# Performance work log

Measured on AMD Instinct MI355X. Metric: run time of the kernel, lower is better.

The kernel has to match this reference:

```python
import jax, jax.numpy as jnp
import numpy as np

CHANNELS = 768
N_HEADS = 12
HEAD_DIM = CHANNELS // N_HEADS
WINDOW = 4
B, T = 4, 1024


def setup_inputs() -> dict:
    key = jax.random.key(0)
    ks = jax.random.split(key, 11)
    C = CHANNELS
    s = 1.0 / np.sqrt(C)
    inp = {
        "x": jax.random.normal(ks[0], (B, C, T), dtype=jnp.float32),
        "w_q": jax.random.normal(ks[1], (C, C), dtype=jnp.float32) * s,
        "b_q": jnp.zeros((C,), dtype=jnp.float32),
        "w_k": jax.random.normal(ks[2], (C, C), dtype=jnp.float32) * s,
        "b_k": jnp.zeros((C,), dtype=jnp.float32),
        "w_v": jax.random.normal(ks[3], (C, C), dtype=jnp.float32) * s,
        "b_v": jnp.zeros((C,), dtype=jnp.float32),
        "w_o": jax.random.normal(ks[4], (C, C), dtype=jnp.float32) * s,
        "b_o": jnp.zeros((C,), dtype=jnp.float32),
        "emb_rel_k": jax.random.normal(ks[5], (2 * WINDOW + 1, HEAD_DIM), dtype=jnp.float32) * 0.01,
        "emb_rel_v": jax.random.normal(ks[6], (2 * WINDOW + 1, HEAD_DIM), dtype=jnp.float32) * 0.01,
    }
    return inp


def _rel_embeddings(emb_k, emb_v, t):
    pos = jnp.arange(t)
    rel_pos = pos[None, :] - pos[:, None]            # (T, T), rel_pos[i,j] = j - i
    outside = jnp.abs(rel_pos) > WINDOW
    rel_idx = jnp.clip(rel_pos, -WINDOW, WINDOW) + WINDOW
    rel_k = jnp.where(outside[:, :, None], 0.0, emb_k[rel_idx])  # (T, T, d)
    rel_v = jnp.where(outside[:, :, None], 0.0, emb_v[rel_idx])
    return rel_k, rel_v


def reference(x, w_q, b_q, w_k, b_k, w_v, b_v, w_o, b_o, emb_rel_k, emb_rel_v):
    Bq, C, t = x.shape
    H, d = N_HEADS, HEAD_DIM
    # 1x1 Conv1d == per-timestep linear over channels
    def proj(w, b):
        return jnp.einsum('oc,bct->bot', w, x) + b[None, :, None]
    # (B, C, T) -> (B, H, T, d)
    def split_heads(y):
        return y.reshape(Bq, H, d, t).transpose(0, 1, 3, 2)
    q = split_heads(proj(w_q, b_q)) / jnp.sqrt(jnp.float32(d))
    k = split_heads(proj(w_k, b_k))
    v = split_heads(proj(w_v, b_v))
    scores = jnp.einsum('bhid,bhjd->bhij', q, k)
    rel_k, rel_v = _rel_embeddings(emb_rel_k, emb_rel_v, t)
    scores = scores + jnp.einsum('bhid,ijd->bhij', q, rel_k)
    attn = jax.nn.softmax(scores, axis=-1)
    out = jnp.einsum('bhij,bhjd->bhid', attn, v)
    out = out + jnp.einsum('bhij,ijd->bhid', attn, rel_v)
    out = out.transpose(0, 1, 3, 2).reshape(Bq, C, t)  # (B, C, T)
    out = jnp.einsum('oc,bct->bot', w_o, out) + b_o[None, :, None]
    return out
```

## Files before the change

kernel.cpp:

```cpp
#include <hip/hip_runtime.h>

#define B_ 4
#define T_ 1024
#define C_ 768
#define H_ 12
#define D_ 64

typedef unsigned short u16;
typedef __attribute__((ext_vector_type(8))) short b16x8;
typedef __attribute__((ext_vector_type(4))) float f32x4;

#define MFMA(a, b, c) __builtin_amdgcn_mfma_f32_16x16x32_bf16(a, b, c, 0, 0, 0)

__device__ __forceinline__ float b2f(u16 u) {
    return __uint_as_float(((unsigned)u) << 16);
}
__device__ __forceinline__ u16 f2b(float f) {
    unsigned u = __float_as_uint(f);
    u += 0x7fffu + ((u >> 16) & 1u);
    return (u16)(u >> 16);
}
__device__ __forceinline__ u16 f2b_tr(float f) {
    return (u16)(__float_as_uint(f) >> 16);
}

__device__ __forceinline__ void g2l16(const u16* g, u16* l) {
    __builtin_amdgcn_global_load_lds(
        (const __attribute__((address_space(1))) unsigned int*)g,
        (__attribute__((address_space(3))) unsigned int*)l, 16, 0, 0);
}

__global__ __launch_bounds__(256) void convw_kernel(
    const float* __restrict__ w0, const float* __restrict__ w1,
    const float* __restrict__ w2, const float* __restrict__ w3,
    u16* __restrict__ o)
{
    const float* src = blockIdx.y == 0 ? w0 : blockIdx.y == 1 ? w1 :
                       blockIdx.y == 2 ? w2 : w3;
    u16* dst = o + (size_t)blockIdx.y * C_ * C_;
    const int i = (blockIdx.x * 256 + threadIdx.x) * 4;
    float4 v = *(const float4*)(src + i);
    ushort4 st = {f2b(v.x), f2b(v.y), f2b(v.z), f2b(v.w)};
    *(ushort4*)(dst + i) = st;
}

__global__ __launch_bounds__(256) void convx_kernel(
    const float* __restrict__ x, u16* __restrict__ xb)
{
    __shared__ u16 tile[64][68];
    const int tid = threadIdx.x;
    const int t0 = blockIdx.x * 64, c0 = blockIdx.y * 64, b = blockIdx.z;
    #pragma unroll
    for (int p = 0; p < 4; ++p) {
        const int cc = p * 16 + (tid >> 4);
        const int t4 = (tid & 15) * 4;
        float4 v = *(const float4*)(x + ((size_t)b * C_ + c0 + cc) * T_ + t0 + t4);
        tile[t4 + 0][cc] = f2b(v.x);
        tile[t4 + 1][cc] = f2b(v.y);
        tile[t4 + 2][cc] = f2b(v.z);
        tile[t4 + 3][cc] = f2b(v.w);
    }
    __syncthreads();
    #pragma unroll
    for (int p = 0; p < 4; ++p) {
        const int tt = p * 16 + (tid >> 4);
        const int c4 = (tid & 15) * 4;
        ushort4 st = *(const ushort4*)&tile[tt][c4];
        *(ushort4*)(xb + ((size_t)b * T_ + t0 + tt) * C_ + c0 + c4) = st;
    }
}

__global__ __launch_bounds__(256) void qkv_mfma_kernel(
    const u16* __restrict__ wb, const u16* __restrict__ xb,
    const float* __restrict__ b_q, const float* __restrict__ b_k,
    const float* __restrict__ b_v,
    u16* __restrict__ q_ws, u16* __restrict__ k_ws, u16* __restrict__ v_ws)
{
    __shared__ __align__(16) u16 a_s[128 * 32];
    __shared__ __align__(16) u16 b_s[128 * 32];

    const int tid = threadIdx.x;
    const int wv = tid >> 6, lane = tid & 63;
    const int lo = lane & 15, quad = lane >> 4;
    const int wm = wv >> 1, wn = wv & 1;
    const int swz = (lo >> 1) & 3;
    const int srow = lane >> 2;
    const int skb  = (lane & 3) ^ ((lane >> 3) & 3);

    const int t0 = blockIdx.x * 128;
    const int mat = blockIdx.y / 6, oy = blockIdx.y % 6;
    const int o0 = oy * 128;
    const int b  = blockIdx.z;

    const u16* A = wb + (size_t)mat * C_ * C_;
    const float* bias = mat == 0 ? b_q : (mat == 1 ? b_k : b_v);
    u16* dst = mat == 0 ? q_ws : (mat == 1 ? k_ws : v_ws);
    const float scale = mat == 0 ? 0.18033688f : 1.0f;

    const size_t bT0 = (size_t)b * T_ + t0;

    f32x4 acc[4][4] = {};

    for (int kk = 0; kk < C_; kk += 32) {
        __syncthreads();
        #pragma unroll
        for (int ia = 0; ia < 2; ++ia) {
            const int row0 = (wv * 2 + ia) * 16;
            g2l16(A + (size_t)(o0 + row0 + srow) * C_ + kk + skb * 8,
                  a_s + row0 * 32);
        }
        #pragma unroll
        for (int ib = 0; ib < 2; ++ib) {
            const int row0 = (wv * 2 + ib) * 16;
            g2l16(xb + (bT0 + row0 + srow) * C_ + kk + skb * 8,
                  b_s + row0 * 32);
        }
        __syncthreads();

        b16x8 af[4], bf[4];
        #pragma unroll
        for (int mi = 0; mi < 4; ++mi) {
            const int m = wm * 64 + mi * 16 + lo;
            af[mi] = *(const b16x8*)(a_s + m * 32 + (quad ^ swz) * 8);
        }
        #pragma unroll
        for (int ni = 0; ni < 4; ++ni) {
            const int n = wn * 64 + ni * 16 + lo;
            bf[ni] = *(const b16x8*)(b_s + n * 32 + (quad ^ swz) * 8);
        }
        #pragma unroll
        for (int mi = 0; mi < 4; ++mi)
            #pragma unroll
            for (int ni = 0; ni < 4; ++ni)
                acc[mi][ni] = MFMA(af[mi], bf[ni], acc[mi][ni]);
    }

    #pragma unroll
    for (int mi = 0; mi < 4; ++mi) {
        const int o_b = o0 + wm * 64 + mi * 16 + quad * 4;
        const float4 bv4 = *(const float4*)(bias + o_b);
        const int h = o_b >> 6;
        const int dd0 = o_b & 63;
        #pragma unroll
        for (int ni = 0; ni < 4; ++ni) {
            const int t = t0 + wn * 64 + ni * 16 + lo;
            f32x4 a = acc[mi][ni];
            ushort4 st;
            st.x = f2b((a[0] + bv4.x) * scale);
            st.y = f2b((a[1] + bv4.y) * scale);
            st.z = f2b((a[2] + bv4.z) * scale);
            st.w = f2b((a[3] + bv4.w) * scale);
            *(ushort4*)(dst + (((size_t)b * H_ + h) * T_ + t) * D_ + dd0) = st;
        }
    }
}

__global__ __launch_bounds__(256) void transv_kernel(
    const u16* __restrict__ src, u16* __restrict__ dst)
{
    __shared__ __align__(16) u16 tile[64 * 72];
    const int tid = threadIdx.x;
    const int t0 = blockIdx.x * 64;
    const int bh = blockIdx.y;
    const u16* s = src + (size_t)bh * T_ * D_;
    u16* d = dst + (size_t)bh * D_ * T_;
    #pragma unroll
    for (int p = 0; p < 2; ++p) {
        const int idx = tid + p * 256;
        const int row = idx >> 3, ch = idx & 7;
        *(b16x8*)(tile + row * 72 + ch * 8) =
            *(const b16x8*)(s + (size_t)(t0 + row) * D_ + ch * 8);
    }
    __syncthreads();
    #pragma unroll
    for (int p = 0; p < 2; ++p) {
        const int idx = tid + p * 256;
        const int dd = idx >> 3, ch = idx & 7;
        union { b16x8 v; u16 e[8]; } t;
        #pragma unroll
        for (int e = 0; e < 8; ++e)
            t.e[e] = tile[(ch * 8 + e) * 72 + dd];
        *(b16x8*)(d + (size_t)dd * T_ + t0 + ch * 8) = t.v;
    }
}

__global__ __launch_bounds__(256) void out_mfma_kernel(
    const u16* __restrict__ wob, const u16* __restrict__ ab,
    const float* __restrict__ bias, float* __restrict__ out)
{
    __shared__ __align__(16) u16 a_s[64 * 32];
    __shared__ __align__(16) u16 b_s[128 * 32];

    const int tid = threadIdx.x;
    const int wv = tid >> 6, lane = tid & 63;
    const int lo = lane & 15, quad = lane >> 4;
    const int wm = wv >> 1, wn = wv & 1;
    const int swz = (lo >> 1) & 3;
    const int srow = lane >> 2;
    const int skb  = (lane & 3) ^ ((lane >> 3) & 3);

    const int t0 = blockIdx.x * 128;
    const int o0 = blockIdx.y * 64;
    const int b  = blockIdx.z;
    const size_t bT0 = (size_t)b * T_ + t0;

    f32x4 acc[2][4] = {};

    for (int kk = 0; kk < C_; kk += 32) {
        __syncthreads();
        {
            const int row0 = wv * 16;
            g2l16(wob + (size_t)(o0 + row0 + srow) * C_ + kk + skb * 8,
                  a_s + row0 * 32);
        }
        #pragma unroll
        for (int ib = 0; ib < 2; ++ib) {
            const int row0 = (wv * 2 + ib) * 16;
            g2l16(ab + (bT0 + row0 + srow) * C_ + kk + skb * 8,
                  b_s + row0 * 32);
        }
        __syncthreads();

        b16x8 af[2], bf[4];
        #pragma unroll
        for (int mi = 0; mi < 2; ++mi) {
            const int m = wm * 32 + mi * 16 + lo;
            af[mi] = *(const b16x8*)(a_s + m * 32 + (quad ^ swz) * 8);
        }
        #pragma unroll
        for (int ni = 0; ni < 4; ++ni) {
            const int n = wn * 64 + ni * 16 + lo;
            bf[ni] = *(const b16x8*)(b_s + n * 32 + (quad ^ swz) * 8);
        }
        #pragma unroll
        for (int mi = 0; mi < 2; ++mi)
            #pragma unroll
            for (int ni = 0; ni < 4; ++ni)
                acc[mi][ni] = MFMA(af[mi], bf[ni], acc[mi][ni]);
    }

    #pragma unroll
    for (int mi = 0; mi < 2; ++mi) {
        const int o_b = o0 + wm * 32 + mi * 16 + quad * 4;
        const float4 bv4 = *(const float4*)(bias + o_b);
        const float bb[4] = {bv4.x, bv4.y, bv4.z, bv4.w};
        #pragma unroll
        for (int ni = 0; ni < 4; ++ni) {
            const int t = t0 + wn * 64 + ni * 16 + lo;
            f32x4 a = acc[mi][ni];
            #pragma unroll
            for (int r = 0; r < 4; ++r)
                out[((size_t)b * C_ + o_b + r) * T_ + t] = a[r] + bb[r];
        }
    }
}

__global__ __launch_bounds__(256, 2) void attn_mfma_kernel(
    const u16* __restrict__ qw, const u16* __restrict__ kw, const u16* __restrict__ vw,
    const float* __restrict__ erk, const float* __restrict__ erv,
    u16* __restrict__ att)
{
    __shared__ __align__(16) u16 k_s[64 * 64];
    __shared__ __align__(16) u16 v_s[64 * 64];
    __shared__ __align__(16) u16 p_s[64 * 64];
    __shared__ float qrel_s[64][9];
    __shared__ float band_s[64][9];
    __shared__ float linv_s[64];

    const int tid = threadIdx.x;
    const int wv = tid >> 6, lane = tid & 63;
    const int lo = lane & 15, quad = lane >> 4;
    const int wi0 = wv * 16;
    const int it0 = blockIdx.x * 64;
    const int h = blockIdx.y, b = blockIdx.z;
    const int bh = b * H_ + h;

    const u16* qp = qw + (size_t)bh * T_ * D_;
    const u16* kp = kw + (size_t)bh * T_ * D_;
    const u16* vp = vw + (size_t)bh * D_ * T_;

    const int srow = lane >> 3;
    const int schunk = (lane & 7) ^ srow;
    const int lsw = lo & 7;

    b16x8 qf[2];
    #pragma unroll
    for (int kc = 0; kc < 2; ++kc)
        qf[kc] = *(const b16x8*)(qp + (size_t)(it0 + wi0 + lo) * D_ + kc * 32 + quad * 8);

    {
        b16x8 ekf[2];
        #pragma unroll
        for (int kc = 0; kc < 2; ++kc) {
            union { b16x8 v; u16 s[8]; } t;
            #pragma unroll
            for (int r = 0; r < 8; ++r) t.s[r] = 0;
            if (lo < 9) {
                const float* e = erk + lo * D_ + kc * 32 + quad * 8;
                #pragma unroll
                for (int r = 0; r < 8; ++r) t.s[r] = f2b(e[r]);
            }
            ekf[kc] = t.v;
        }
        f32x4 acc = {};
        acc = MFMA(qf[0], ekf[0], acc);
        acc = MFMA(qf[1], ekf[1], acc);
        if (lo < 9)
            #pragma unroll
            for (int r = 0; r < 4; ++r)
                qrel_s[wi0 + quad * 4 + r][lo] = acc[r];
    }

    for (int idx = lane; idx < 16 * 9; idx += 64)
        band_s[wi0 + idx / 9][idx % 9] = -1e30f;

    f32x4 o[4] = {};
    float lpart = 0.f;

    for (int jt = 0; jt < T_; jt += 64) {
        __syncthreads();
        #pragma unroll
        for (int i2 = 0; i2 < 2; ++i2) {
            const int row0 = (wv * 2 + i2) * 8;
            g2l16(kp + (size_t)(jt + row0 + srow) * D_ + schunk * 8, k_s + row0 * 64);
            g2l16(vp + (size_t)(row0 + srow) * T_ + jt + schunk * 8, v_s + row0 * 64);
        }
        __syncthreads();

        f32x4 st[4];
        #pragma unroll
        for (int mt = 0; mt < 4; ++mt) {
            const int kr = mt * 16 + lo;
            const b16x8 ka0 = *(const b16x8*)(k_s + kr * 64 + ((quad) ^ lsw) * 8);
            const b16x8 ka1 = *(const b16x8*)(k_s + kr * 64 + ((4 + quad) ^ lsw) * 8);
            f32x4 a = {};
            a = MFMA(ka0, qf[0], a);
            a = MFMA(ka1, qf[1], a);
            st[mt] = a;
        }

        if (jt >= it0 - 67 && jt <= it0 + 67) {
            const int ibase = it0 + wi0 + lo;
            #pragma unroll
            for (int mt = 0; mt < 4; ++mt)
                #pragma unroll
                for (int r = 0; r < 4; ++r) {
                    const int rr = (jt + mt * 16 + quad * 4 + r) - ibase + 4;
                    if (rr >= 0 && rr <= 8) {
                        const float s2 = st[mt][r] + qrel_s[wi0 + lo][rr];
                        st[mt][r] = s2;
                        band_s[wi0 + lo][rr] = s2;
                    }
                }
        }

        #pragma unroll
        for (int mt = 0; mt < 4; ++mt)
            #pragma unroll
            for (int r = 0; r < 4; ++r) {
                const float e = exp2f(st[mt][r]);
                st[mt][r] = e;
                lpart += e;
            }

        #pragma unroll
        for (int mt = 0; mt < 4; ++mt) {
            ushort4 pw;
            pw.x = f2b_tr(st[mt][0]);
            pw.y = f2b_tr(st[mt][1]);
            pw.z = f2b_tr(st[mt][2]);
            pw.w = f2b_tr(st[mt][3]);
            const int slot = (mt * 2 + (quad >> 1)) ^ lsw;
            *(ushort4*)(p_s + (wi0 + lo) * 64 + slot * 8 + (quad & 1) * 4) = pw;
        }

        const b16x8 pa0 = *(const b16x8*)(p_s + (wi0 + lo) * 64 + ((quad) ^ lsw) * 8);
        const b16x8 pa1 = *(const b16x8*)(p_s + (wi0 + lo) * 64 + ((4 + quad) ^ lsw) * 8);
        #pragma unroll
        for (int nd = 0; nd < 4; ++nd) {
            const int vr = nd * 16 + lo;
            const b16x8 vb0 = *(const b16x8*)(v_s + vr * 64 + ((quad) ^ lsw) * 8);
            const b16x8 vb1 = *(const b16x8*)(v_s + vr * 64 + ((4 + quad) ^ lsw) * 8);
            o[nd] = MFMA(pa0, vb0, o[nd]);
            o[nd] = MFMA(pa1, vb1, o[nd]);
        }
    }

    {
        union { b16x8 v; u16 s[8]; } tb;
        #pragma unroll
        for (int r = 0; r < 8; ++r) {
            const int rr = quad * 8 + r;
            tb.s[r] = (rr <= 8) ? f2b(exp2f(band_s[wi0 + lo][rr])) : (u16)0;
        }
        const b16x8 baf = tb.v;
        #pragma unroll
        for (int nd = 0; nd < 4; ++nd) {
            union { b16x8 v; u16 s[8]; } t;
            #pragma unroll
            for (int r = 0; r < 8; ++r) {
                const int rr = quad * 8 + r;
                t.s[r] = (rr <= 8) ? f2b(erv[rr * D_ + nd * 16 + lo]) : (u16)0;
            }
            o[nd] = MFMA(baf, t.v, o[nd]);
        }
    }

    lpart += __shfl_xor(lpart, 16);
    lpart += __shfl_xor(lpart, 32);
    if (quad == 0) linv_s[wi0 + lo] = 1.f / lpart;
    #pragma unroll
    for (int r = 0; r < 4; ++r) {
        const int il = wi0 + quad * 4 + r;
        const float inv = linv_s[il];
        const size_t base = ((size_t)b * T_ + it0 + il) * C_ + h * D_;
        #pragma unroll
        for (int nd = 0; nd < 4; ++nd)
            att[base + nd * 16 + lo] = f2b(o[nd][r] * inv);
    }
}

extern "C" void kernel_launch(void* const* d_in, const int* in_sizes, int n_in,
                              void* d_out, int out_size, void* d_ws, size_t ws_size,
                              hipStream_t stream) {
    const float* x   = (const float*)d_in[0];
    const float* w_q = (const float*)d_in[1];
    const float* b_q = (const float*)d_in[2];
    const float* w_k = (const float*)d_in[3];
    const float* b_k = (const float*)d_in[4];
    const float* w_v = (const float*)d_in[5];
    const float* b_v = (const float*)d_in[6];
    const float* w_o = (const float*)d_in[7];
    const float* b_o = (const float*)d_in[8];
    const float* erk = (const float*)d_in[9];
    const float* erv = (const float*)d_in[10];

    const size_t N = (size_t)B_ * C_ * T_;
    u16* q_ws  = (u16*)d_ws;
    u16* k_ws  = q_ws + N;
    u16* vraw  = q_ws + 2 * N;
    u16* vdT   = q_ws + 3 * N;
    u16* xb    = q_ws + 4 * N;
    u16* a_ws  = vraw;
    u16* wb    = q_ws + 5 * N;
    float* out = (float*)d_out;

    dim3 blk(256, 1, 1);

    convw_kernel<<<dim3(C_ * C_ / 1024, 4), blk, 0, stream>>>(w_q, w_k, w_v, w_o, wb);
    convx_kernel<<<dim3(T_ / 64, C_ / 64, B_), blk, 0, stream>>>(x, xb);

    qkv_mfma_kernel<<<dim3(T_ / 128, 18, B_), blk, 0, stream>>>(
        wb, xb, b_q, b_k, b_v, q_ws, k_ws, vraw);

    transv_kernel<<<dim3(T_ / 64, H_ * B_), blk, 0, stream>>>(vraw, vdT);

    attn_mfma_kernel<<<dim3(T_ / 64, H_, B_), blk, 0, stream>>>(
        q_ws, k_ws, vdT, erk, erv, a_ws);

    out_mfma_kernel<<<dim3(T_ / 128, C_ / 64, B_), blk, 0, stream>>>(
        wb + 3 * (size_t)C_ * C_, a_ws, b_o, out);
}
```

Baseline: 170.2 us.

## Fuse conversion kernels, fold V transpose into QKV epilogue, enlarge out-proj tile

Merges the weight and input bf16 conversion kernels into one launch. The V transpose moves into the QKV GEMM epilogue, which stages the tile in shared memory and writes the transposed layout directly, removing the separate transpose kernel and its extra global round trip. The output projection tile grows from 64 to 128 output channels per block, which raises reuse but halves the grid to 192 blocks. The larger QKV shared buffer (128x136) may lower occupancy.

Result: slower. 176.0 us (+3.4%).

```diff
diff --git a/kernel.cpp b/kernel.cpp
--- a/kernel.cpp
+++ b/kernel.cpp
@@ -30,26 +30,30 @@
         (__attribute__((address_space(3))) unsigned int*)l, 16, 0, 0);
 }
 
-__global__ __launch_bounds__(256) void convw_kernel(
+__global__ __launch_bounds__(256) void conv_fused_kernel(
     const float* __restrict__ w0, const float* __restrict__ w1,
     const float* __restrict__ w2, const float* __restrict__ w3,
-    u16* __restrict__ o)
-{
-    const float* src = blockIdx.y == 0 ? w0 : blockIdx.y == 1 ? w1 :
-                       blockIdx.y == 2 ? w2 : w3;
-    u16* dst = o + (size_t)blockIdx.y * C_ * C_;
-    const int i = (blockIdx.x * 256 + threadIdx.x) * 4;
-    float4 v = *(const float4*)(src + i);
-    ushort4 st = {f2b(v.x), f2b(v.y), f2b(v.z), f2b(v.w)};
-    *(ushort4*)(dst + i) = st;
-}
-
-__global__ __launch_bounds__(256) void convx_kernel(
-    const float* __restrict__ x, u16* __restrict__ xb)
+    u16* __restrict__ wb, const float* __restrict__ x, u16* __restrict__ xb)
 {
     __shared__ u16 tile[64][68];
+    const int bx = blockIdx.x;
     const int tid = threadIdx.x;
-    const int t0 = blockIdx.x * 64, c0 = blockIdx.y * 64, b = blockIdx.z;
+
+    if (bx < 2304) {
+        const int mat = bx / 576;
+        const float* src = mat == 0 ? w0 : mat == 1 ? w1 : mat == 2 ? w2 : w3;
+        u16* dst = wb + (size_t)mat * C_ * C_;
+        const int i = ((bx % 576) * 256 + tid) * 4;
+        float4 v = *(const float4*)(src + i);
+        ushort4 st = {f2b(v.x), f2b(v.y), f2b(v.z), f2b(v.w)};
+        *(ushort4*)(dst + i) = st;
+        return;
+    }
+
+    const int cx = bx - 2304;
+    const int t0 = (cx & 15) * 64;
+    const int c0 = ((cx >> 4) % 12) * 64;
+    const int b  = cx / 192;
     #pragma unroll
     for (int p = 0; p < 4; ++p) {
         const int cc = p * 16 + (tid >> 4);
@@ -74,10 +78,11 @@
     const u16* __restrict__ wb, const u16* __restrict__ xb,
     const float* __restrict__ b_q, const float* __restrict__ b_k,
     const float* __restrict__ b_v,
-    u16* __restrict__ q_ws, u16* __restrict__ k_ws, u16* __restrict__ v_ws)
+    u16* __restrict__ q_ws, u16* __restrict__ k_ws, u16* __restrict__ vT_ws)
 {
-    __shared__ __align__(16) u16 a_s[128 * 32];
-    __shared__ __align__(16) u16 b_s[128 * 32];
+    __shared__ __align__(16) u16 smem[128 * 136];
+    u16* a_s = smem;
+    u16* b_s = smem + 128 * 32;
 
     const int tid = threadIdx.x;
     const int wv = tid >> 6, lane = tid & 63;
@@ -94,7 +99,6 @@
 
     const u16* A = wb + (size_t)mat * C_ * C_;
     const float* bias = mat == 0 ? b_q : (mat == 1 ? b_k : b_v);
-    u16* dst = mat == 0 ? q_ws : (mat == 1 ? k_ws : v_ws);
     const float scale = mat == 0 ? 0.18033688f : 1.0f;
 
     const size_t bT0 = (size_t)b * T_ + t0;
@@ -135,52 +139,52 @@
                 acc[mi][ni] = MFMA(af[mi], bf[ni], acc[mi][ni]);
     }
 
-    #pragma unroll
-    for (int mi = 0; mi < 4; ++mi) {
-        const int o_b = o0 + wm * 64 + mi * 16 + quad * 4;
-        const float4 bv4 = *(const float4*)(bias + o_b);
-        const int h = o_b >> 6;
-        const int dd0 = o_b & 63;
-        #pragma unroll
-        for (int ni = 0; ni < 4; ++ni) {
-            const int t = t0 + wn * 64 + ni * 16 + lo;
-            f32x4 a = acc[mi][ni];
-            ushort4 st;
-            st.x = f2b((a[0] + bv4.x) * scale);
-            st.y = f2b((a[1] + bv4.y) * scale);
-            st.z = f2b((a[2] + bv4.z) * scale);
-            st.w = f2b((a[3] + bv4.w) * scale);
-            *(ushort4*)(dst + (((size_t)b * H_ + h) * T_ + t) * D_ + dd0) = st;
-        }
-    }
-}
-
-__global__ __launch_bounds__(256) void transv_kernel(
-    const u16* __restrict__ src, u16* __restrict__ dst)
-{
-    __shared__ __align__(16) u16 tile[64 * 72];
-    const int tid = threadIdx.x;
-    const int t0 = blockIdx.x * 64;
-    const int bh = blockIdx.y;
-    const u16* s = src + (size_t)bh * T_ * D_;
-    u16* d = dst + (size_t)bh * D_ * T_;
-    #pragma unroll
-    for (int p = 0; p < 2; ++p) {
-        const int idx = tid + p * 256;
-        const int row = idx >> 3, ch = idx & 7;
-        *(b16x8*)(tile + row * 72 + ch * 8) =
-            *(const b16x8*)(s + (size_t)(t0 + row) * D_ + ch * 8);
-    }
-    __syncthreads();
-    #pragma unroll
-    for (int p = 0; p < 2; ++p) {
-        const int idx = tid + p * 256;
-        const int dd = idx >> 3, ch = idx & 7;
-        union { b16x8 v; u16 e[8]; } t;
-        #pragma unroll
-        for (int e = 0; e < 8; ++e)
-            t.e[e] = tile[(ch * 8 + e) * 72 + dd];
-        *(b16x8*)(d + (size_t)dd * T_ + t0 + ch * 8) = t.v;
+    if (mat != 2) {
+        u16* dst = mat == 0 ? q_ws : k_ws;
+        #pragma unroll
+        for (int mi = 0; mi < 4; ++mi) {
+            const int o_b = o0 + wm * 64 + mi * 16 + quad * 4;
+            const float4 bv4 = *(const float4*)(bias + o_b);
+            const int h = o_b >> 6;
+            const int dd0 = o_b & 63;
+            #pragma unroll
+            for (int ni = 0; ni < 4; ++ni) {
+                const int t = t0 + wn * 64 + ni * 16 + lo;
+                f32x4 a = acc[mi][ni];
+                ushort4 st;
+                st.x = f2b((a[0] + bv4.x) * scale);
+                st.y = f2b((a[1] + bv4.y) * scale);
+                st.z = f2b((a[2] + bv4.z) * scale);
+                st.w = f2b((a[3] + bv4.w) * scale);
+                *(ushort4*)(dst + (((size_t)b * H_ + h) * T_ + t) * D_ + dd0) = st;
+            }
+        }
+    } else {
+        u16* vt = smem;
+        __syncthreads();
+        #pragma unroll
+        for (int mi = 0; mi < 4; ++mi) {
+            const int o_l = wm * 64 + mi * 16 + quad * 4;
+            const float4 bv4 = *(const float4*)(bias + o0 + o_l);
+            const float bb[4] = {bv4.x, bv4.y, bv4.z, bv4.w};
+            #pragma unroll
+            for (int ni = 0; ni < 4; ++ni) {
+                const int t_l = wn * 64 + ni * 16 + lo;
+                #pragma unroll
+                for (int r = 0; r < 4; ++r)
+                    vt[(o_l + r) * 136 + t_l] = f2b(acc[mi][ni][r] + bb[r]);
+            }
+        }
+        __syncthreads();
+        #pragma unroll
+        for (int c = 0; c < 8; ++c) {
+            const int idx = c * 256 + tid;
+            const int row = idx >> 4, ch = idx & 15;
+            const b16x8 val = *(const b16x8*)(vt + row * 136 + ch * 8);
+            const int o_g = o0 + row;
+            const int h = o_g >> 6, dd = o_g & 63;
+            *(b16x8*)(vT_ws + (((size_t)b * H_ + h) * D_ + dd) * T_ + t0 + ch * 8) = val;
+        }
     }
 }
 
@@ -188,7 +192,7 @@
     const u16* __restrict__ wob, const u16* __restrict__ ab,
     const float* __restrict__ bias, float* __restrict__ out)
 {
-    __shared__ __align__(16) u16 a_s[64 * 32];
+    __shared__ __align__(16) u16 a_s[128 * 32];
     __shared__ __align__(16) u16 b_s[128 * 32];
 
     const int tid = threadIdx.x;
@@ -200,16 +204,17 @@
     const int skb  = (lane & 3) ^ ((lane >> 3) & 3);
 
     const int t0 = blockIdx.x * 128;
-    const int o0 = blockIdx.y * 64;
+    const int o0 = blockIdx.y * 128;
     const int b  = blockIdx.z;
     const size_t bT0 = (size_t)b * T_ + t0;
 
-    f32x4 acc[2][4] = {};
+    f32x4 acc[4][4] = {};
 
     for (int kk = 0; kk < C_; kk += 32) {
         __syncthreads();
-        {
-            const int row0 = wv * 16;
+        #pragma unroll
+        for (int ia = 0; ia < 2; ++ia) {
+            const int row0 = (wv * 2 + ia) * 16;
             g2l16(wob + (size_t)(o0 + row0 + srow) * C_ + kk + skb * 8,
                   a_s + row0 * 32);
         }
@@ -221,10 +226,10 @@
         }
         __syncthreads();
 
-        b16x8 af[2], bf[4];
-        #pragma unroll
-        for (int mi = 0; mi < 2; ++mi) {
-            const int m = wm * 32 + mi * 16 + lo;
+        b16x8 af[4], bf[4];
+        #pragma unroll
+        for (int mi = 0; mi < 4; ++mi) {
+            const int m = wm * 64 + mi * 16 + lo;
             af[mi] = *(const b16x8*)(a_s + m * 32 + (quad ^ swz) * 8);
         }
         #pragma unroll
@@ -233,15 +238,15 @@
             bf[ni] = *(const b16x8*)(b_s + n * 32 + (quad ^ swz) * 8);
         }
         #pragma unroll
-        for (int mi = 0; mi < 2; ++mi)
+        for (int mi = 0; mi < 4; ++mi)
             #pragma unroll
             for (int ni = 0; ni < 4; ++ni)
                 acc[mi][ni] = MFMA(af[mi], bf[ni], acc[mi][ni]);
     }
 
     #pragma unroll
-    for (int mi = 0; mi < 2; ++mi) {
-        const int o_b = o0 + wm * 32 + mi * 16 + quad * 4;
+    for (int mi = 0; mi < 4; ++mi) {
+        const int o_b = o0 + wm * 64 + mi * 16 + quad * 4;
         const float4 bv4 = *(const float4*)(bias + o_b);
         const float bb[4] = {bv4.x, bv4.y, bv4.z, bv4.w};
         #pragma unroll
@@ -438,26 +443,22 @@
     const size_t N = (size_t)B_ * C_ * T_;
     u16* q_ws  = (u16*)d_ws;
     u16* k_ws  = q_ws + N;
-    u16* vraw  = q_ws + 2 * N;
+    u16* a_ws  = q_ws + 2 * N;
     u16* vdT   = q_ws + 3 * N;
     u16* xb    = q_ws + 4 * N;
-    u16* a_ws  = vraw;
     u16* wb    = q_ws + 5 * N;
     float* out = (float*)d_out;
 
     dim3 blk(256, 1, 1);
 
-    convw_kernel<<<dim3(C_ * C_ / 1024, 4), blk, 0, stream>>>(w_q, w_k, w_v, w_o, wb);
-    convx_kernel<<<dim3(T_ / 64, C_ / 64, B_), blk, 0, stream>>>(x, xb);
+    conv_fused_kernel<<<dim3(3072), blk, 0, stream>>>(w_q, w_k, w_v, w_o, wb, x, xb);
 
     qkv_mfma_kernel<<<dim3(T_ / 128, 18, B_), blk, 0, stream>>>(
-        wb, xb, b_q, b_k, b_v, q_ws, k_ws, vraw);
-
-    transv_kernel<<<dim3(T_ / 64, H_ * B_), blk, 0, stream>>>(vraw, vdT);
+        wb, xb, b_q, b_k, b_v, q_ws, k_ws, vdT);
 
     attn_mfma_kernel<<<dim3(T_ / 64, H_, B_), blk, 0, stream>>>(
         q_ws, k_ws, vdT, erk, erv, a_ws);
 
-    out_mfma_kernel<<<dim3(T_ / 128, C_ / 64, B_), blk, 0, stream>>>(
+    out_mfma_kernel<<<dim3(T_ / 128, C_ / 128, B_), blk, 0, stream>>>(
         wb + 3 * (size_t)C_ * C_, a_ws, b_o, out);
 }
```
